# Optimization experiments

Measured on AMD Instinct MI355X. Metric: run time of the kernel, lower is better.

The kernel has to match this reference:

```python
import jax, jax.numpy as jnp
import numpy as np

EPS = 1e-5


def conv2d(x, w, b, stride=1, pad=1):
    out = jax.lax.conv_general_dilated(
        x, w, (stride, stride), [(pad, pad), (pad, pad)],
        dimension_numbers=('NCHW', 'OIHW', 'NCHW'))
    return out + b[None, :, None, None]


def bn_inf(x, gamma, beta, mean, var):
    inv = gamma / jnp.sqrt(var + EPS)
    return x * inv[None, :, None, None] + (beta - mean * inv)[None, :, None, None]


def deform_conv(x, offset, weight, stride, pad, dil):
    # x: [B,Ci,H,W], offset: [B,2*K*K,Ho,Wo] (dy,dx interleaved per kernel pos),
    # weight: [Co,Ci,K,K]. torchvision DeformConv2d v1 semantics, no bias.
    B, Ci, H, W = x.shape
    Co, _, K, _ = weight.shape
    KK = K * K
    Ho = (H + 2 * pad - dil * (K - 1) - 1) // stride + 1
    Wo = (W + 2 * pad - dil * (K - 1) - 1) // stride + 1
    dy = offset[:, 0::2]  # [B,KK,Ho,Wo]
    dx = offset[:, 1::2]
    ky, kx = jnp.meshgrid(jnp.arange(K), jnp.arange(K), indexing='ij')
    ky = ky.reshape(KK).astype(x.dtype)
    kx = kx.reshape(KK).astype(x.dtype)
    base_y = (jnp.arange(Ho) * stride - pad).astype(x.dtype)
    base_x = (jnp.arange(Wo) * stride - pad).astype(x.dtype)
    ys = base_y[None, None, :, None] + (ky * dil)[None, :, None, None] + dy
    xs = base_x[None, None, None, :] + (kx * dil)[None, :, None, None] + dx
    y0 = jnp.floor(ys)
    x0 = jnp.floor(xs)
    fy = ys - y0
    fx = xs - x0

    def gather(img, iy, ix):
        # img: [Ci,H,W]; iy, ix: [KK,Ho,Wo] float integer-valued coords
        valid = (iy >= 0) & (iy < H) & (ix >= 0) & (ix < W)
        iyc = jnp.clip(iy, 0, H - 1).astype(jnp.int32)
        ixc = jnp.clip(ix, 0, W - 1).astype(jnp.int32)
        v = img[:, iyc, ixc]  # [Ci,KK,Ho,Wo]
        return v * valid[None].astype(img.dtype)

    def sample_one(img, y0b, x0b, fyb, fxb):
        w00 = (1 - fyb) * (1 - fxb)
        w01 = (1 - fyb) * fxb
        w10 = fyb * (1 - fxb)
        w11 = fyb * fxb
        s = (gather(img, y0b, x0b) * w00[None]
             + gather(img, y0b, x0b + 1) * w01[None]
             + gather(img, y0b + 1, x0b) * w10[None]
             + gather(img, y0b + 1, x0b + 1) * w11[None])
        return s  # [Ci,KK,Ho,Wo]

    sampled = jax.vmap(sample_one)(x, y0, x0, fy, fx)  # [B,Ci,KK,Ho,Wo]
    return jnp.einsum('oik,bikhw->bohw', weight.reshape(Co, Ci, KK), sampled)


def setup_inputs() -> dict:
    key = jax.random.key(0)
    ks = jax.random.split(key, 16)
    B, C, H, W = 8, 128, 64, 64
    d = dict(
        x=jax.random.normal(ks[0], (B, C, H, W), jnp.float32),
        w_off1=jax.random.normal(ks[1], (18, C, 3, 3), jnp.float32) * 0.01,
        b_off1=jnp.zeros((18,), jnp.float32),
        w_dc1=jax.random.normal(ks[2], (C, C, 3, 3), jnp.float32) * 0.05,
        g1=jnp.ones((C,), jnp.float32),
        beta1=jnp.zeros((C,), jnp.float32),
        m1=jax.random.normal(ks[3], (C,), jnp.float32) * 0.1,
        v1=jax.random.uniform(ks[4], (C,), jnp.float32) + 0.5,
        w_off2=jax.random.normal(ks[5], (18, C, 3, 3), jnp.float32) * 0.01,
        b_off2=jnp.zeros((18,), jnp.float32),
        w_dc2=jax.random.normal(ks[6], (C, C, 3, 3), jnp.float32) * 0.05,
        g2=jnp.ones((C,), jnp.float32),
        beta2=jnp.zeros((C,), jnp.float32),
        m2=jax.random.normal(ks[7], (C,), jnp.float32) * 0.1,
        v2=jax.random.uniform(ks[8], (C,), jnp.float32) + 0.5,
    )
    return d


def reference(x, w_off1, b_off1, w_dc1, g1, beta1, m1, v1,
              w_off2, b_off2, w_dc2, g2, beta2, m2, v2):
    # BasicBlock6 forward (stride=1, in_planes==planes => identity shortcut)
    off1 = conv2d(x, w_off1, b_off1, stride=1, pad=1)
    out = jax.nn.relu(bn_inf(deform_conv(x, off1, w_dc1, 1, 2, 2), g1, beta1, m1, v1))
    off2 = conv2d(out, w_off2, b_off2, stride=1, pad=1)
    out = bn_inf(deform_conv(out, off2, w_dc2, 1, 2, 2), g2, beta2, m2, v2)
    out = out + x  # identity shortcut
    return jax.nn.relu(out)
```

## Files before the change

### kernel.cpp

```cpp
#include <hip/hip_runtime.h>
#include <hip/hip_bf16.h>

#define CH   128
#define HH   64
#define WW   64
#define OFFC 18

typedef __attribute__((ext_vector_type(8))) short bf16x8;
typedef __attribute__((ext_vector_type(4))) short bf16x4;
typedef __attribute__((ext_vector_type(4))) float f32x4;

static __device__ __forceinline__ unsigned short f2bf(float f) {
    __hip_bfloat16 h = __float2bfloat16(f);
    return *reinterpret_cast<unsigned short*>(&h);
}
static __device__ __forceinline__ float bf2f(unsigned short u) {
    union { unsigned int i; float f; } x; x.i = ((unsigned int)u) << 16;
    return x.f;
}
static __device__ __forceinline__ float2 pk_mul2(float2 a, float2 b) {
    float2 d;
    asm("v_pk_mul_f32 %0, %1, %2" : "=v"(d) : "v"(a), "v"(b));
    return d;
}
static __device__ __forceinline__ float2 pk_fma2(float2 a, float2 b, float2 c) {
    float2 d;
    asm("v_pk_fma_f32 %0, %1, %2, %3" : "=v"(d) : "v"(a), "v"(b), "v"(c));
    return d;
}
static __device__ __forceinline__ float2 bf2f2(unsigned int d) {
    float2 u;
    u.x = __uint_as_float(d << 16);
    u.y = __uint_as_float(d & 0xffff0000u);
    return u;
}

__global__ __launch_bounds__(256) void prep_kernel(
    const float* __restrict__ x, unsigned short* __restrict__ xh,
    const float* __restrict__ wdc1, const float* __restrict__ wdc2,
    const float* __restrict__ wof1, const float* __restrict__ wof2,
    unsigned short* __restrict__ wpk1, unsigned short* __restrict__ wpk2,
    unsigned short* __restrict__ wpo1, unsigned short* __restrict__ wpo2)
{
    __shared__ float s[CH][WW + 1];
    int blk = blockIdx.x;
    int tid = threadIdx.x;

    if (blk < 1152) {
        const float* w = (blk < 576) ? wdc1 : wdc2;
        unsigned short* wp = (blk < 576) ? wpk1 : wpk2;
        int id = (blk % 576) * 256 + tid;
        int j    = id & 7;
        int lane = (id >> 3) & 63;
        int ot   = (id >> 9) & 7;
        int kk   = (id >> 12) & 3;
        int k    = id >> 14;
        int o = ot * 16 + (lane & 15);
        int i = kk * 32 + (lane >> 4) * 8 + j;
        wp[id] = f2bf(w[(o * CH + i) * 9 + k]);
        return;
    }
    if (blk < 1440) {
        const float* w = (blk < 1296) ? wof1 : wof2;
        unsigned short* wp = (blk < 1296) ? wpo1 : wpo2;
        int id = ((blk - 1152) % 144) * 256 + tid;
        int j    = id & 7;
        int lane = (id >> 3) & 63;
        int mt   = (id >> 9) & 1;
        int kk   = (id >> 10) & 3;
        int k    = id >> 12;
        int o = mt * 16 + (lane & 15);
        int i = kk * 32 + (lane >> 4) * 8 + j;
        wp[id] = (o < OFFC) ? f2bf(w[(o * CH + i) * 9 + k]) : (unsigned short)0;
        return;
    }

    int nb = blk - 1440;
    const float* xb = x + ((size_t)(nb >> 6) * CH * HH + (nb & 63)) * WW;

    int c_off = tid >> 4, w0 = (tid & 15) * 4;
    #pragma unroll
    for (int it = 0; it < 8; ++it) {
        int c = it * 16 + c_off;
        float4 vv = *(const float4*)&xb[(size_t)c * HH * WW + w0];
        s[c][w0] = vv.x; s[c][w0 + 1] = vv.y; s[c][w0 + 2] = vv.z; s[c][w0 + 3] = vv.w;
    }
    __syncthreads();

    int w = tid & 63, c0 = (tid >> 6) * 32;
    unsigned short* dst = xh + ((size_t)nb * WW + w) * CH + c0;
    unsigned short tmp[32];
    #pragma unroll
    for (int j = 0; j < 32; ++j) tmp[j] = f2bf(s[c0 + j][w]);
    #pragma unroll
    for (int q = 0; q < 4; ++q)
        *(bf16x8*)(dst + q * 8) = *(const bf16x8*)(tmp + q * 8);
}

__global__ __launch_bounds__(256) void off_conv_mfma_kernel(
    const unsigned short* __restrict__ xh,
    const unsigned short* __restrict__ wpo,
    const float* __restrict__ bias,
    unsigned short* __restrict__ offh)
{
    int wgid = blockIdx.x;
    int blk  = (wgid & 7) * 64 + (wgid >> 3);
    int b = blk >> 6, oh = blk & 63;
    int tid = threadIdx.x;
    int lane = tid & 63;
    int nt = tid >> 6;
    int nl = lane & 15;
    int kg = lane >> 4;

    f32x4 acc0 = {0.f, 0.f, 0.f, 0.f}, acc1 = {0.f, 0.f, 0.f, 0.f};
    const unsigned short* xb = xh + (size_t)b * HH * WW * CH;

    for (int k = 0; k < 9; ++k) {
        int ky = k / 3, kx = k - ky * 3;
        int ih = oh - 1 + ky;
        if (ih < 0 || ih >= HH) continue;
        int iw = nt * 16 + nl + kx - 1;
        bool valid = (iw >= 0) && (iw < WW);
        const unsigned short* row = xb + ((size_t)ih * WW + (valid ? iw : 0)) * CH + kg * 8;
        const unsigned short* wk = wpo + (size_t)k * 4096;
        #pragma unroll
        for (int kk = 0; kk < 4; ++kk) {
            bf16x8 bfrag = {0, 0, 0, 0, 0, 0, 0, 0};
            if (valid) bfrag = *(const bf16x8*)(row + kk * 32);
            bf16x8 a0 = *(const bf16x8*)(wk + (kk * 2 + 0) * 512 + lane * 8);
            bf16x8 a1 = *(const bf16x8*)(wk + (kk * 2 + 1) * 512 + lane * 8);
            acc0 = __builtin_amdgcn_mfma_f32_16x16x32_bf16(a0, bfrag, acc0, 0, 0, 0);
            acc1 = __builtin_amdgcn_mfma_f32_16x16x32_bf16(a1, bfrag, acc1, 0, 0, 0);
        }
    }

    int ow = nt * 16 + nl;
    #pragma unroll
    for (int r = 0; r < 4; ++r) {
        int co = kg * 4 + r;
        offh[(((size_t)b * OFFC + co) * HH + oh) * WW + ow] = f2bf(acc0[r] + bias[co]);
    }
    if (kg == 0) {
        #pragma unroll
        for (int r = 0; r < 2; ++r) {
            int co = 16 + r;
            offh[(((size_t)b * OFFC + co) * HH + oh) * WW + ow] = f2bf(acc1[r] + bias[co]);
        }
    }
}

#define P_COORD(K, OW, CW, PTR) do {                                          \
    int ky_ = (K) / 3, kx_ = (K) - ky_ * 3;                                   \
    float dy_ = off_s[2 * (K)][OW];                                           \
    float dx_ = off_s[2 * (K) + 1][OW];                                       \
    float ys_ = (float)(oh - 2 + ky_ * 2) + dy_;                              \
    float xs_ = (float)((OW) - 2 + kx_ * 2) + dx_;                            \
    float y0f_ = floorf(ys_), x0f_ = floorf(xs_);                             \
    float fy_ = ys_ - y0f_, fx_ = xs_ - x0f_;                                 \
    int y0_ = (int)y0f_, x0_ = (int)x0f_;                                     \
    int y1_ = y0_ + 1, x1_ = x0_ + 1;                                         \
    bool vy0_ = (y0_ >= 0) & (y0_ < HH), vy1_ = (y1_ >= 0) & (y1_ < HH);      \
    bool vx0_ = (x0_ >= 0) & (x0_ < WW), vx1_ = (x1_ >= 0) & (x1_ < WW);      \
    int y0c_ = min(max(y0_, 0), HH - 1), y1c_ = min(max(y1_, 0), HH - 1);     \
    int x0c_ = min(max(x0_, 0), WW - 1), x1c_ = min(max(x1_, 0), WW - 1);     \
    CW[0] = (1.f - fy_) * (1.f - fx_) * ((vy0_ && vx0_) ? 1.f : 0.f);         \
    CW[1] = (1.f - fy_) * fx_         * ((vy0_ && vx1_) ? 1.f : 0.f);         \
    CW[2] = fy_ * (1.f - fx_)         * ((vy1_ && vx0_) ? 1.f : 0.f);         \
    CW[3] = fy_ * fx_                 * ((vy1_ && vx1_) ? 1.f : 0.f);         \
    PTR[0] = xb + ((size_t)(y0c_ * WW + x0c_)) * CH + cig * 8;                \
    PTR[1] = xb + ((size_t)(y0c_ * WW + x1c_)) * CH + cig * 8;                \
    PTR[2] = xb + ((size_t)(y1c_ * WW + x0c_)) * CH + cig * 8;                \
    PTR[3] = xb + ((size_t)(y1c_ * WW + x1c_)) * CH + cig * 8;                \
} while (0)

#define P_ISSUE(PTR, LD) do {                                                 \
    _Pragma("unroll")                                                         \
    for (int c_ = 0; c_ < 4; ++c_) {                                          \
        LD[0][c_] = *(const bf16x8*)(PTR[c_]);                                \
        LD[1][c_] = *(const bf16x8*)(PTR[c_] + 64);                           \
    }                                                                         \
} while (0)

#define P_BLEND(OW, CW, LD, BUF) do {                                         \
    int swz_ = ((OW) & 7) << 4;                                               \
    float2 cw0p_ = make_float2(CW[0], CW[0]);                                 \
    float2 cw1p_ = make_float2(CW[1], CW[1]);                                 \
    float2 cw2p_ = make_float2(CW[2], CW[2]);                                 \
    float2 cw3p_ = make_float2(CW[3], CW[3]);                                 \
    _Pragma("unroll")                                                         \
    for (int q_ = 0; q_ < 2; ++q_) {                                          \
        const unsigned int* d0_ = (const unsigned int*)&LD[q_][0];            \
        const unsigned int* d1_ = (const unsigned int*)&LD[q_][1];            \
        const unsigned int* d2_ = (const unsigned int*)&LD[q_][2];            \
        const unsigned int* d3_ = (const unsigned int*)&LD[q_][3];            \
        union { bf16x8 v8; unsigned short u[8]; } wu_;                        \
        _Pragma("unroll")                                                     \
        for (int p_ = 0; p_ < 4; ++p_) {                                      \
            float2 r_ = pk_mul2(cw0p_, bf2f2(d0_[p_]));                       \
            r_ = pk_fma2(cw1p_, bf2f2(d1_[p_]), r_);                          \
            r_ = pk_fma2(cw2p_, bf2f2(d2_[p_]), r_);                          \
            r_ = pk_fma2(cw3p_, bf2f2(d3_[p_]), r_);                          \
            wu_.u[2 * p_]     = f2bf(r_.x);                                   \
            wu_.u[2 * p_ + 1] = f2bf(r_.y);                                   \
        }                                                                     \
        int byte_ = ((OW) * 256 + (q_ * 64 + cig * 8) * 2) ^ swz_;            \
        *(bf16x8*)((char*)sB[BUF] + byte_) = wu_.v8;                          \
    }                                                                         \
} while (0)

#define C_PREF(K, AP) do {                                                    \
    const unsigned short* wk_ = wpk + (size_t)(K) * 16384;                    \
    _Pragma("unroll")                                                         \
    for (int kk_ = 0; kk_ < 4; ++kk_) {                                       \
        AP[kk_ * 2 + 0] = *(const bf16x8*)(wk_ + (size_t)(kk_ * 8 + 2 * cwi)     * 512 + lane * 8); \
        AP[kk_ * 2 + 1] = *(const bf16x8*)(wk_ + (size_t)(kk_ * 8 + 2 * cwi + 1) * 512 + lane * 8); \
    }                                                                         \
} while (0)

__global__ __launch_bounds__(512, 4) void deform_pc_kernel(
    const unsigned short* __restrict__ xh,
    const unsigned short* __restrict__ offh,
    const unsigned short* __restrict__ wpk,
    const float* __restrict__ g, const float* __restrict__ beta,
    const float* __restrict__ m, const float* __restrict__ v,
    const float* __restrict__ residual,
    unsigned short* __restrict__ out_h,
    float* __restrict__ out_f)
{
    __shared__ unsigned short sB[2][64 * 128];
    __shared__ float off_s[OFFC][WW];
    __shared__ int flg[4];

    int wgid = blockIdx.x;
    int blk  = (wgid & 7) * 64 + (wgid >> 3);
    int b = blk >> 6, oh = blk & 63;
    int tid = threadIdx.x, lane = tid & 63, wv = tid >> 6;

    const unsigned short* xb = xh + (size_t)b * HH * WW * CH;

    for (int i = tid; i < OFFC * WW; i += 512) {
        int co = i >> 6, owl = i & 63;
        off_s[co][owl] =
            bf2f(offh[(((size_t)b * OFFC + co) * HH + oh) * WW + owl]);
    }
    if (tid < 4) flg[tid] = 0;
    __syncthreads();

    if (wv < 4) {
        int s_ow = tid >> 3;
        int cig  = tid & 7;

        float cwA[4], cwB[4];
        const unsigned short *ptA[4], *ptB[4];
        bf16x8 ldA[2][4], ldB[2][4];

        P_COORD(0, s_ow, cwA, ptA);
        P_COORD(0, s_ow + 32, cwB, ptB);
        P_ISSUE(ptA, ldA);
        P_ISSUE(ptB, ldB);

        for (int k = 0; k < 9; ++k) {
            int buf = k & 1;
            if (k >= 2) {
                int tgt = 4 * (k >> 1);
                while (__hip_atomic_load(&flg[2 + buf], __ATOMIC_ACQUIRE,
                                         __HIP_MEMORY_SCOPE_WORKGROUP) < tgt)
                    __builtin_amdgcn_s_sleep(1);
            }
            P_BLEND(s_ow,      cwA, ldA, buf);
            P_BLEND(s_ow + 32, cwB, ldB, buf);
            asm volatile("s_waitcnt lgkmcnt(0)" ::: "memory");
            if (lane == 0)
                __hip_atomic_fetch_add(&flg[buf], 1, __ATOMIC_RELEASE,
                                       __HIP_MEMORY_SCOPE_WORKGROUP);
            if (k < 8) {
                P_COORD(k + 1, s_ow, cwA, ptA);
                P_COORD(k + 1, s_ow + 32, cwB, ptB);
                P_ISSUE(ptA, ldA);
                P_ISSUE(ptB, ldB);
            }
        }
    } else {
        int cwi = wv - 4;
        f32x4 acc[2][4];
        #pragma unroll
        for (int a = 0; a < 2; ++a)
            #pragma unroll
            for (int q = 0; q < 4; ++q) acc[a][q] = (f32x4){0.f, 0.f, 0.f, 0.f};

        bf16x8 aP[8];
        C_PREF(0, aP);

        for (int k = 0; k < 9; ++k) {
            int buf = k & 1;
            int tgt = 4 * ((k >> 1) + 1);
            while (__hip_atomic_load(&flg[buf], __ATOMIC_ACQUIRE,
                                     __HIP_MEMORY_SCOPE_WORKGROUP) < tgt)
                __builtin_amdgcn_s_sleep(1);

            __builtin_amdgcn_s_setprio(1);
            #pragma unroll
            for (int kk = 0; kk < 4; ++kk) {
                #pragma unroll
                for (int owt = 0; owt < 4; ++owt) {
                    int owl = owt * 16 + (lane & 15);
                    int rbyte = (owl * 256 + (kk * 32 + (lane >> 4) * 8) * 2)
                                ^ ((owl & 7) << 4);
                    bf16x8 bfv = *(const bf16x8*)((const char*)sB[buf] + rbyte);
                    acc[0][owt] = __builtin_amdgcn_mfma_f32_16x16x32_bf16(
                                      aP[kk * 2 + 0], bfv, acc[0][owt], 0, 0, 0);
                    acc[1][owt] = __builtin_amdgcn_mfma_f32_16x16x32_bf16(
                                      aP[kk * 2 + 1], bfv, acc[1][owt], 0, 0, 0);
                }
            }
            __builtin_amdgcn_s_setprio(0);
            asm volatile("s_waitcnt lgkmcnt(0)" ::: "memory");
            if (lane == 0)
                __hip_atomic_fetch_add(&flg[2 + buf], 1, __ATOMIC_RELEASE,
                                       __HIP_MEMORY_SCOPE_WORKGROUP);
            if (k < 8) C_PREF(k + 1, aP);
        }

        #pragma unroll
        for (int otl = 0; otl < 2; ++otl) {
            int ob = (2 * cwi + otl) * 16 + (lane >> 4) * 4;
            float inv[4], sh[4];
            #pragma unroll
            for (int r = 0; r < 4; ++r) {
                int o = ob + r;
                float iv = g[o] / sqrtf(v[o] + 1e-5f);
                inv[r] = iv; sh[r] = beta[o] - m[o] * iv;
            }
            if (out_h != nullptr) {
                #pragma unroll
                for (int owt = 0; owt < 4; ++owt) {
                    int ow = owt * 16 + (lane & 15);
                    union { bf16x4 v4; unsigned short u[4]; } pk;
                    #pragma unroll
                    for (int r = 0; r < 4; ++r) {
                        float val = acc[otl][owt][r] * inv[r] + sh[r];
                        pk.u[r] = f2bf(fmaxf(val, 0.f));
                    }
                    *(bf16x4*)(out_h + ((size_t)(b * HH + oh) * WW + ow) * CH + ob) = pk.v4;
                }
            } else {
                #pragma unroll
                for (int r = 0; r < 4; ++r) {
                    int o = ob + r;
                    #pragma unroll
                    for (int owt = 0; owt < 4; ++owt) {
                        int ow = owt * 16 + (lane & 15);
                        size_t idx = (((size_t)b * CH + o) * HH + oh) * WW + ow;
                        float val = acc[otl][owt][r] * inv[r] + sh[r] + residual[idx];
                        out_f[idx] = fmaxf(val, 0.f);
                    }
                }
            }
        }
    }
}

extern "C" void kernel_launch(void* const* d_in, const int* in_sizes, int n_in,
                              void* d_out, int out_size, void* d_ws, size_t ws_size,
                              hipStream_t stream)
{
    const float* x      = (const float*)d_in[0];
    const float* w_off1 = (const float*)d_in[1];
    const float* b_off1 = (const float*)d_in[2];
    const float* w_dc1  = (const float*)d_in[3];
    const float* g1     = (const float*)d_in[4];
    const float* beta1  = (const float*)d_in[5];
    const float* m1     = (const float*)d_in[6];
    const float* v1     = (const float*)d_in[7];
    const float* w_off2 = (const float*)d_in[8];
    const float* b_off2 = (const float*)d_in[9];
    const float* w_dc2  = (const float*)d_in[10];
    const float* g2     = (const float*)d_in[11];
    const float* beta2  = (const float*)d_in[12];
    const float* m2     = (const float*)d_in[13];
    const float* v2     = (const float*)d_in[14];
    float* out = (float*)d_out;

    char* ws = (char*)d_ws;
    unsigned short* xh    = (unsigned short*)ws;
    unsigned short* out1h = (unsigned short*)(ws + 8388608);
    unsigned short* offh  = (unsigned short*)(ws + 16777216);
    unsigned short* wpk1  = (unsigned short*)(ws + 17956864);
    unsigned short* wpk2  = (unsigned short*)(ws + 18251776);
    unsigned short* wpo1  = (unsigned short*)(ws + 18546688);
    unsigned short* wpo2  = (unsigned short*)(ws + 18620416);

    prep_kernel<<<1952, 256, 0, stream>>>(x, xh, w_dc1, w_dc2, w_off1, w_off2,
                                          wpk1, wpk2, wpo1, wpo2);

    off_conv_mfma_kernel<<<512, 256, 0, stream>>>(xh, wpo1, b_off1, offh);
    deform_pc_kernel<<<512, 512, 0, stream>>>(xh, offh, wpk1,
                                              g1, beta1, m1, v1,
                                              nullptr, out1h, nullptr);
    off_conv_mfma_kernel<<<512, 256, 0, stream>>>(out1h, wpo2, b_off2, offh);
    deform_pc_kernel<<<512, 512, 0, stream>>>(out1h, offh, wpk2,
                                              g2, beta2, m2, v2,
                                              x, nullptr, out);
}
```

Before: 90.92 us.

## Split deformable conv workgroups into half-rows with 256 threads and direct weight loads

Each deformable-conv workgroup now covers half an output row (32 columns) with 4 waves instead of a full row with 8, doubling the grid to 1024 workgroups. Producer lanes now each gather 32 channels for one column instead of 8 channels for two columns. Consumer waves compute 4 output-channel tiles by 2 column tiles and load weight fragments straight from global memory inside the MFMA loop, replacing the register prefetch of the next tap. This aims for better occupancy and load balance, but each weight fragment is now reused over half as many columns and weight-load latency sits directly in the MFMA loop.

Result: slower. 110.9 us (+21.9%).

```diff
diff --git a/kernel.cpp b/kernel.cpp
--- a/kernel.cpp
+++ b/kernel.cpp
@@ -149,12 +149,13 @@
     }
 }
 
-#define P_COORD(K, OW, CW, PTR) do {                                          \
-    int ky_ = (K) / 3, kx_ = (K) - ky_ * 3;                                   \
-    float dy_ = off_s[2 * (K)][OW];                                           \
-    float dx_ = off_s[2 * (K) + 1][OW];                                       \
+#define P_COORD(K) do {                                                       \
+    int k_ = (K);                                                             \
+    int ky_ = k_ / 3, kx_ = k_ - ky_ * 3;                                     \
+    float dy_ = off_s[2 * k_][s_ow];                                          \
+    float dx_ = off_s[2 * k_ + 1][s_ow];                                      \
     float ys_ = (float)(oh - 2 + ky_ * 2) + dy_;                              \
-    float xs_ = (float)((OW) - 2 + kx_ * 2) + dx_;                            \
+    float xs_ = (float)(ow_g - 2 + kx_ * 2) + dx_;                            \
     float y0f_ = floorf(ys_), x0f_ = floorf(xs_);                             \
     float fy_ = ys_ - y0f_, fx_ = xs_ - x0f_;                                 \
     int y0_ = (int)y0f_, x0_ = (int)x0f_;                                     \
@@ -163,61 +164,53 @@
     bool vx0_ = (x0_ >= 0) & (x0_ < WW), vx1_ = (x1_ >= 0) & (x1_ < WW);      \
     int y0c_ = min(max(y0_, 0), HH - 1), y1c_ = min(max(y1_, 0), HH - 1);     \
     int x0c_ = min(max(x0_, 0), WW - 1), x1c_ = min(max(x1_, 0), WW - 1);     \
-    CW[0] = (1.f - fy_) * (1.f - fx_) * ((vy0_ && vx0_) ? 1.f : 0.f);         \
-    CW[1] = (1.f - fy_) * fx_         * ((vy0_ && vx1_) ? 1.f : 0.f);         \
-    CW[2] = fy_ * (1.f - fx_)         * ((vy1_ && vx0_) ? 1.f : 0.f);         \
-    CW[3] = fy_ * fx_                 * ((vy1_ && vx1_) ? 1.f : 0.f);         \
-    PTR[0] = xb + ((size_t)(y0c_ * WW + x0c_)) * CH + cig * 8;                \
-    PTR[1] = xb + ((size_t)(y0c_ * WW + x1c_)) * CH + cig * 8;                \
-    PTR[2] = xb + ((size_t)(y1c_ * WW + x0c_)) * CH + cig * 8;                \
-    PTR[3] = xb + ((size_t)(y1c_ * WW + x1c_)) * CH + cig * 8;                \
+    cw[0] = (1.f - fy_) * (1.f - fx_) * ((vy0_ && vx0_) ? 1.f : 0.f);         \
+    cw[1] = (1.f - fy_) * fx_         * ((vy0_ && vx1_) ? 1.f : 0.f);         \
+    cw[2] = fy_ * (1.f - fx_)         * ((vy1_ && vx0_) ? 1.f : 0.f);         \
+    cw[3] = fy_ * fx_                 * ((vy1_ && vx1_) ? 1.f : 0.f);         \
+    pt[0] = xb + ((size_t)(y0c_ * WW + x0c_)) * CH + ci0;                     \
+    pt[1] = xb + ((size_t)(y0c_ * WW + x1c_)) * CH + ci0;                     \
+    pt[2] = xb + ((size_t)(y1c_ * WW + x0c_)) * CH + ci0;                     \
+    pt[3] = xb + ((size_t)(y1c_ * WW + x1c_)) * CH + ci0;                     \
 } while (0)
 
-#define P_ISSUE(PTR, LD) do {                                                 \
+#define P_ISSUE() do {                                                        \
     _Pragma("unroll")                                                         \
     for (int c_ = 0; c_ < 4; ++c_) {                                          \
-        LD[0][c_] = *(const bf16x8*)(PTR[c_]);                                \
-        LD[1][c_] = *(const bf16x8*)(PTR[c_] + 64);                           \
+        _Pragma("unroll")                                                     \
+        for (int h_ = 0; h_ < 4; ++h_)                                        \
+            ld[c_][h_] = *(const bf16x8*)(pt[c_] + h_ * 8);                   \
     }                                                                         \
 } while (0)
 
-#define P_BLEND(OW, CW, LD, BUF) do {                                         \
-    int swz_ = ((OW) & 7) << 4;                                               \
-    float2 cw0p_ = make_float2(CW[0], CW[0]);                                 \
-    float2 cw1p_ = make_float2(CW[1], CW[1]);                                 \
-    float2 cw2p_ = make_float2(CW[2], CW[2]);                                 \
-    float2 cw3p_ = make_float2(CW[3], CW[3]);                                 \
+#define P_BLEND(BUF) do {                                                     \
+    int swz_ = (s_ow & 7) << 4;                                               \
+    float2 c0p_ = make_float2(cw[0], cw[0]);                                  \
+    float2 c1p_ = make_float2(cw[1], cw[1]);                                  \
+    float2 c2p_ = make_float2(cw[2], cw[2]);                                  \
+    float2 c3p_ = make_float2(cw[3], cw[3]);                                  \
     _Pragma("unroll")                                                         \
-    for (int q_ = 0; q_ < 2; ++q_) {                                          \
-        const unsigned int* d0_ = (const unsigned int*)&LD[q_][0];            \
-        const unsigned int* d1_ = (const unsigned int*)&LD[q_][1];            \
-        const unsigned int* d2_ = (const unsigned int*)&LD[q_][2];            \
-        const unsigned int* d3_ = (const unsigned int*)&LD[q_][3];            \
+    for (int h_ = 0; h_ < 4; ++h_) {                                          \
+        const unsigned int* d0_ = (const unsigned int*)&ld[0][h_];            \
+        const unsigned int* d1_ = (const unsigned int*)&ld[1][h_];            \
+        const unsigned int* d2_ = (const unsigned int*)&ld[2][h_];            \
+        const unsigned int* d3_ = (const unsigned int*)&ld[3][h_];            \
         union { bf16x8 v8; unsigned short u[8]; } wu_;                        \
         _Pragma("unroll")                                                     \
         for (int p_ = 0; p_ < 4; ++p_) {                                      \
-            float2 r_ = pk_mul2(cw0p_, bf2f2(d0_[p_]));                       \
-            r_ = pk_fma2(cw1p_, bf2f2(d1_[p_]), r_);                          \
-            r_ = pk_fma2(cw2p_, bf2f2(d2_[p_]), r_);                          \
-            r_ = pk_fma2(cw3p_, bf2f2(d3_[p_]), r_);                          \
+            float2 r_ = pk_mul2(c0p_, bf2f2(d0_[p_]));                        \
+            r_ = pk_fma2(c1p_, bf2f2(d1_[p_]), r_);                           \
+            r_ = pk_fma2(c2p_, bf2f2(d2_[p_]), r_);                           \
+            r_ = pk_fma2(c3p_, bf2f2(d3_[p_]), r_);                           \
             wu_.u[2 * p_]     = f2bf(r_.x);                                   \
             wu_.u[2 * p_ + 1] = f2bf(r_.y);                                   \
         }                                                                     \
-        int byte_ = ((OW) * 256 + (q_ * 64 + cig * 8) * 2) ^ swz_;            \
+        int byte_ = (s_ow * 256 + ci0 * 2 + h_ * 16) ^ swz_;                  \
         *(bf16x8*)((char*)sB[BUF] + byte_) = wu_.v8;                          \
     }                                                                         \
 } while (0)
 
-#define C_PREF(K, AP) do {                                                    \
-    const unsigned short* wk_ = wpk + (size_t)(K) * 16384;                    \
-    _Pragma("unroll")                                                         \
-    for (int kk_ = 0; kk_ < 4; ++kk_) {                                       \
-        AP[kk_ * 2 + 0] = *(const bf16x8*)(wk_ + (size_t)(kk_ * 8 + 2 * cwi)     * 512 + lane * 8); \
-        AP[kk_ * 2 + 1] = *(const bf16x8*)(wk_ + (size_t)(kk_ * 8 + 2 * cwi + 1) * 512 + lane * 8); \
-    }                                                                         \
-} while (0)
-
-__global__ __launch_bounds__(512, 4) void deform_pc_kernel(
+__global__ __launch_bounds__(256, 4) void deform_pc_kernel(
     const unsigned short* __restrict__ xh,
     const unsigned short* __restrict__ offh,
     const unsigned short* __restrict__ wpk,
@@ -227,90 +220,91 @@
     unsigned short* __restrict__ out_h,
     float* __restrict__ out_f)
 {
-    __shared__ unsigned short sB[2][64 * 128];
-    __shared__ float off_s[OFFC][WW];
+    __shared__ unsigned short sB[2][32 * 128];
+    __shared__ float off_s[OFFC][32];
     __shared__ int flg[4];
 
     int wgid = blockIdx.x;
-    int blk  = (wgid & 7) * 64 + (wgid >> 3);
-    int b = blk >> 6, oh = blk & 63;
+    int blk  = (wgid & 7) * 128 + (wgid >> 3);
+    int owh = blk & 1, oh = (blk >> 1) & 63, b = blk >> 7;
+    int ow0 = owh * 32;
     int tid = threadIdx.x, lane = tid & 63, wv = tid >> 6;
 
     const unsigned short* xb = xh + (size_t)b * HH * WW * CH;
 
-    for (int i = tid; i < OFFC * WW; i += 512) {
-        int co = i >> 6, owl = i & 63;
+    for (int i = tid; i < OFFC * 32; i += 256) {
+        int co = i >> 5, owl = i & 31;
         off_s[co][owl] =
-            bf2f(offh[(((size_t)b * OFFC + co) * HH + oh) * WW + owl]);
+            bf2f(offh[(((size_t)b * OFFC + co) * HH + oh) * WW + ow0 + owl]);
     }
     if (tid < 4) flg[tid] = 0;
     __syncthreads();
 
-    if (wv < 4) {
-        int s_ow = tid >> 3;
-        int cig  = tid & 7;
-
-        float cwA[4], cwB[4];
-        const unsigned short *ptA[4], *ptB[4];
-        bf16x8 ldA[2][4], ldB[2][4];
-
-        P_COORD(0, s_ow, cwA, ptA);
-        P_COORD(0, s_ow + 32, cwB, ptB);
-        P_ISSUE(ptA, ldA);
-        P_ISSUE(ptB, ldB);
+    if (wv < 2) {
+        int s_ow = tid >> 2;
+        int cq   = tid & 3;
+        int ci0  = cq * 32;
+        int ow_g = ow0 + s_ow;
+
+        float cw[4];
+        const unsigned short* pt[4];
+        bf16x8 ld[4][4];
+
+        P_COORD(0); P_ISSUE();
 
         for (int k = 0; k < 9; ++k) {
             int buf = k & 1;
             if (k >= 2) {
-                int tgt = 4 * (k >> 1);
+                int tgt = 2 * (k >> 1);
                 while (__hip_atomic_load(&flg[2 + buf], __ATOMIC_ACQUIRE,
                                          __HIP_MEMORY_SCOPE_WORKGROUP) < tgt)
                     __builtin_amdgcn_s_sleep(1);
             }
-            P_BLEND(s_ow,      cwA, ldA, buf);
-            P_BLEND(s_ow + 32, cwB, ldB, buf);
+            P_BLEND(buf);
             asm volatile("s_waitcnt lgkmcnt(0)" ::: "memory");
             if (lane == 0)
                 __hip_atomic_fetch_add(&flg[buf], 1, __ATOMIC_RELEASE,
                                        __HIP_MEMORY_SCOPE_WORKGROUP);
-            if (k < 8) {
-                P_COORD(k + 1, s_ow, cwA, ptA);
-                P_COORD(k + 1, s_ow + 32, cwB, ptB);
-                P_ISSUE(ptA, ldA);
-                P_ISSUE(ptB, ldB);
-            }
+            if (k < 8) { P_COORD(k + 1); P_ISSUE(); }
         }
     } else {
-        int cwi = wv - 4;
-        f32x4 acc[2][4];
+        int cwi = wv - 2;
+        f32x4 acc[4][2];
         #pragma unroll
-        for (int a = 0; a < 2; ++a)
+        for (int a = 0; a < 4; ++a)
             #pragma unroll
-            for (int q = 0; q < 4; ++q) acc[a][q] = (f32x4){0.f, 0.f, 0.f, 0.f};
-
-        bf16x8 aP[8];
-        C_PREF(0, aP);
+            for (int q = 0; q < 2; ++q) acc[a][q] = (f32x4){0.f, 0.f, 0.f, 0.f};
 
         for (int k = 0; k < 9; ++k) {
             int buf = k & 1;
-            int tgt = 4 * ((k >> 1) + 1);
+            int tgt = 2 * ((k >> 1) + 1);
             while (__hip_atomic_load(&flg[buf], __ATOMIC_ACQUIRE,
                                      __HIP_MEMORY_SCOPE_WORKGROUP) < tgt)
                 __builtin_amdgcn_s_sleep(1);
 
+            const unsigned short* wk = wpk + (size_t)k * 16384;
             __builtin_amdgcn_s_setprio(1);
             #pragma unroll
             for (int kk = 0; kk < 4; ++kk) {
+                bf16x8 bf0, bf1;
+                {
+                    int owl0 = (lane & 15);
+                    int owl1 = 16 + (lane & 15);
+                    int rb0 = (owl0 * 256 + (kk * 32 + (lane >> 4) * 8) * 2)
+                              ^ ((owl0 & 7) << 4);
+                    int rb1 = (owl1 * 256 + (kk * 32 + (lane >> 4) * 8) * 2)
+                              ^ ((owl1 & 7) << 4);
+                    bf0 = *(const bf16x8*)((const char*)sB[buf] + rb0);
+                    bf1 = *(const bf16x8*)((const char*)sB[buf] + rb1);
+                }
                 #pragma unroll
-                for (int owt = 0; owt < 4; ++owt) {
-                    int owl = owt * 16 + (lane & 15);
-                    int rbyte = (owl * 256 + (kk * 32 + (lane >> 4) * 8) * 2)
-                                ^ ((owl & 7) << 4);
-                    bf16x8 bfv = *(const bf16x8*)((const char*)sB[buf] + rbyte);
-                    acc[0][owt] = __builtin_amdgcn_mfma_f32_16x16x32_bf16(
-                                      aP[kk * 2 + 0], bfv, acc[0][owt], 0, 0, 0);
-                    acc[1][owt] = __builtin_amdgcn_mfma_f32_16x16x32_bf16(
-                                      aP[kk * 2 + 1], bfv, acc[1][owt], 0, 0, 0);
+                for (int otl = 0; otl < 4; ++otl) {
+                    bf16x8 a = *(const bf16x8*)(
+                        wk + (size_t)(kk * 8 + 4 * cwi + otl) * 512 + lane * 8);
+                    acc[otl][0] = __builtin_amdgcn_mfma_f32_16x16x32_bf16(
+                                      a, bf0, acc[otl][0], 0, 0, 0);
+                    acc[otl][1] = __builtin_amdgcn_mfma_f32_16x16x32_bf16(
+                                      a, bf1, acc[otl][1], 0, 0, 0);
                 }
             }
             __builtin_amdgcn_s_setprio(0);
@@ -318,12 +312,11 @@
             if (lane == 0)
                 __hip_atomic_fetch_add(&flg[2 + buf], 1, __ATOMIC_RELEASE,
                                        __HIP_MEMORY_SCOPE_WORKGROUP);
-            if (k < 8) C_PREF(k + 1, aP);
         }
 
         #pragma unroll
-        for (int otl = 0; otl < 2; ++otl) {
-            int ob = (2 * cwi + otl) * 16 + (lane >> 4) * 4;
+        for (int otl = 0; otl < 4; ++otl) {
+            int ob = (4 * cwi + otl) * 16 + (lane >> 4) * 4;
             float inv[4], sh[4];
             #pragma unroll
             for (int r = 0; r < 4; ++r) {
@@ -333,8 +326,8 @@
             }
             if (out_h != nullptr) {
                 #pragma unroll
-                for (int owt = 0; owt < 4; ++owt) {
-                    int ow = owt * 16 + (lane & 15);
+                for (int owt = 0; owt < 2; ++owt) {
+                    int ow = ow0 + owt * 16 + (lane & 15);
                     union { bf16x4 v4; unsigned short u[4]; } pk;
                     #pragma unroll
                     for (int r = 0; r < 4; ++r) {
@@ -348,8 +341,8 @@
                 for (int r = 0; r < 4; ++r) {
                     int o = ob + r;
                     #pragma unroll
-                    for (int owt = 0; owt < 4; ++owt) {
-                        int ow = owt * 16 + (lane & 15);
+                    for (int owt = 0; owt < 2; ++owt) {
+                        int ow = ow0 + owt * 16 + (lane & 15);
                         size_t idx = (((size_t)b * CH + o) * HH + oh) * WW + ow;
                         float val = acc[otl][owt][r] * inv[r] + sh[r] + residual[idx];
                         out_f[idx] = fmaxf(val, 0.f);
@@ -394,11 +387,11 @@
                                           wpk1, wpk2, wpo1, wpo2);
 
     off_conv_mfma_kernel<<<512, 256, 0, stream>>>(xh, wpo1, b_off1, offh);
-    deform_pc_kernel<<<512, 512, 0, stream>>>(xh, offh, wpk1,
-                                              g1, beta1, m1, v1,
-                                              nullptr, out1h, nullptr);
+    deform_pc_kernel<<<1024, 256, 0, stream>>>(xh, offh, wpk1,
+                                               g1, beta1, m1, v1,
+                                               nullptr, out1h, nullptr);
     off_conv_mfma_kernel<<<512, 256, 0, stream>>>(out1h, wpo2, b_off2, offh);
-    deform_pc_kernel<<<512, 512, 0, stream>>>(out1h, offh, wpk2,
-                                              g2, beta2, m2, v2,
-                                              x, nullptr, out);
-}
+    deform_pc_kernel<<<1024, 256, 0, stream>>>(out1h, offh, wpk2,
+                                               g2, beta2, m2, v2,
+                                               x, nullptr, out);
+}
```
